# Performance work log

Measured on AMD Instinct MI355X. Metric: run time of the kernel, lower is better.

The kernel has to match this reference:

```python
import jax, jax.numpy as jnp
import numpy as np
from jax import lax

EPS = 1e-5

def binarize(x):
    # sign forward, straight-through (identity) backward, matching torch .data-trick Binarize
    return x + lax.stop_gradient(jnp.sign(x) - x)

def conv2d(x, w, pad):
    return lax.conv_general_dilated(x, w, window_strides=(1, 1),
                                    padding=[(pad, pad), (pad, pad)],
                                    dimension_numbers=('NCHW', 'OIHW', 'NCHW'))

def maxpool_k2s1(x):
    return lax.reduce_window(x, -jnp.inf, lax.max, (1, 1, 2, 2), (1, 1, 1, 1), 'VALID')

def batchnorm(x, g, b):
    # training-mode BN: batch statistics over (N, H, W)
    mean = jnp.mean(x, axis=(0, 2, 3), keepdims=True)
    var = jnp.var(x, axis=(0, 2, 3), keepdims=True)
    return (x - mean) * lax.rsqrt(var + EPS) * g[None, :, None, None] + b[None, :, None, None]

def hardtanh(x):
    return jnp.clip(x, -1.0, 1.0)

def setup_inputs() -> dict:
    key = jax.random.key(0)
    ks = jax.random.split(key, 11)
    B = 4096
    return {
        'x':   jax.random.normal(ks[0], (B, 12, 12, 15), jnp.float32),
        'w1':  jax.random.normal(ks[1], (48, 12, 3, 3), jnp.float32) * 0.1,
        'g1':  1.0 + 0.1 * jax.random.normal(ks[2], (48,), jnp.float32),
        'b1':  0.1 * jax.random.normal(ks[3], (48,), jnp.float32),
        'w2':  jax.random.normal(ks[4], (48, 48, 3, 3), jnp.float32) * 0.1,
        'g2':  1.0 + 0.1 * jax.random.normal(ks[5], (48,), jnp.float32),
        'b2':  0.1 * jax.random.normal(ks[6], (48,), jnp.float32),
        'w3':  jax.random.normal(ks[7], (48, 48, 3, 3), jnp.float32) * 0.1,
        'g3':  1.0 + 0.1 * jax.random.normal(ks[8], (48,), jnp.float32),
        'b3':  0.1 * jax.random.normal(ks[9], (48,), jnp.float32),
        'wfc': jax.random.normal(ks[10], (5, 54 * 48), jnp.float32) * 0.02,
    }

def reference(x, w1, g1, b1, w2, g2, b2, w3, g3, b3, wfc):
    # BinarizeConv2d binarizes activations (in_channels != 3) and weights; returns binarized input too
    xb1 = binarize(x)                                  # [B,12,12,15]
    h = conv2d(xb1, binarize(w1), pad=1)               # [B,48,12,15]
    h = maxpool_k2s1(h)                                # [B,48,11,14]
    h = hardtanh(batchnorm(h, g1, b1))
    xb2 = binarize(h)
    h = conv2d(xb2, binarize(w2), pad=0)               # [B,48,9,12]
    h = hardtanh(batchnorm(h, g2, b2))
    xb3 = binarize(h)
    h = conv2d(xb3, binarize(w3), pad=0)               # [B,48,7,10]
    h = maxpool_k2s1(h)                                # [B,48,6,9] -> 54 spatial
    h = hardtanh(batchnorm(h, g3, b3))
    f = h.reshape(h.shape[0], -1)                      # [B, 2592]
    fb = binarize(f)
    out = fb @ binarize(wfc).T                         # [B, 5]  (LogSoftmax defined but never applied)
    return (out, xb1, xb2, xb3, fb)
```

## Files before the change

### kernel.cpp

```cpp
#include <hip/hip_runtime.h>
#include <stdint.h>

typedef unsigned long long u64;
typedef unsigned short u16;


#define NB 4096

#define WS_STATS 0
#define WS_W1P   20480
#define WS_W2P   24576
#define WS_W3P   28672
#define WS_WFCP  32768
#define WS_A1    40960
#define WS_P1    5111808

#define OUT_OFF 0
#define XB1_OFF 20480
#define XB2_OFF 8867840
#define XB3_OFF 39145472
#define FB_OFF  60379136

__device__ __forceinline__ float fsign(float v) {
    return (v > 0.0f) ? 1.0f : ((v < 0.0f) ? -1.0f : 0.0f);
}

__global__ __launch_bounds__(512)
void kw_pack(const float* __restrict__ w1, const float* __restrict__ w2,
             const float* __restrict__ w3, const float* __restrict__ wfc,
             char* __restrict__ ws) {
    int t = threadIdx.x;
    long long* stats = (long long*)(ws + WS_STATS);
    for (int i = t; i < 2304; i += 512) stats[i] = 0;
    if (t < 432) {
        int oc = t / 9, p = t % 9;
        u16 m1 = 0;
        for (int c = 0; c < 12; ++c)
            if (w1[oc*108 + c*9 + p] > 0.0f) m1 |= (u16)(1u << c);
        ((u16*)(ws + WS_W1P))[t] = m1;
        u64 m2 = 0, m3 = 0;
        for (int c = 0; c < 48; ++c) {
            if (w2[oc*432 + c*9 + p] > 0.0f) m2 |= (1ull << c);
            if (w3[oc*432 + c*9 + p] > 0.0f) m3 |= (1ull << c);
        }
        ((u64*)(ws + WS_W2P))[t] = m2;
        ((u64*)(ws + WS_W3P))[t] = m3;
    }
    if (t < 205) {
        int o = t / 41, j = t % 41;
        u64 m = 0;
        for (int l = 0; l < 64; ++l) {
            int k = j*64 + l;
            if (k < 2592 && wfc[o*2592 + k] > 0.0f) m |= (1ull << l);
        }
        ((u64*)(ws + WS_WFCP))[t] = m;
    }
}

__global__ __launch_bounds__(256)
void k0_binx(const float* __restrict__ x, float* __restrict__ dout,
             char* __restrict__ ws) {
    int id = blockIdx.x*256 + threadIdx.x;
    int b = id / 45, s4 = id % 45;
    const float4* xp = (const float4*)(x + b*2160);
    float4* op = (float4*)(dout + XB1_OFF + (size_t)b*2160);
    u16 m0 = 0, m1 = 0, m2 = 0, m3 = 0;
    #pragma unroll
    for (int c = 0; c < 12; ++c) {
        float4 v = xp[c*45 + s4];
        float4 o;
        o.x = fsign(v.x); o.y = fsign(v.y); o.z = fsign(v.z); o.w = fsign(v.w);
        op[c*45 + s4] = o;
        u16 bit = (u16)(1u << c);
        if (v.x > 0.0f) m0 |= bit;
        if (v.y > 0.0f) m1 |= bit;
        if (v.z > 0.0f) m2 |= bit;
        if (v.w > 0.0f) m3 |= bit;
    }
    ushort4 mm; mm.x = m0; mm.y = m1; mm.z = m2; mm.w = m3;
    *((ushort4*)((u16*)(ws + WS_A1) + b*180 + s4*4)) = mm;
}

__global__ __launch_bounds__(256)
void k1_conv1(char* __restrict__ ws) {
    __shared__ u16 As[180];
    __shared__ u16 Wsh[432];
    __shared__ int cmap_i[2160];
    __shared__ int pl_i[1848];
    signed char* cmap = (signed char*)cmap_i;
    signed char* pl = (signed char*)pl_i;
    int t = threadIdx.x, b = blockIdx.x;
    const u16* A1 = (const u16*)(ws + WS_A1);
    const u16* W1p = (const u16*)(ws + WS_W1P);
    if (t < 180) As[t] = A1[b*180 + t];
    for (int i = t; i < 432; i += 256) Wsh[i] = W1p[i];
    __syncthreads();
    for (int i4 = t; i4 < 2160; i4 += 256) {
        int r = 0;
        #pragma unroll
        for (int u = 0; u < 4; ++u) {
            int i = i4*4 + u;
            int oc = i / 180, s = i % 180, y = s / 15, xx = s % 15;
            int acc = 0, valid = 0;
            #pragma unroll
            for (int ky = 0; ky < 3; ++ky) {
                int yy = y + ky - 1;
                if (yy < 0 || yy >= 12) continue;
                #pragma unroll
                for (int kx = 0; kx < 3; ++kx) {
                    int xc = xx + kx - 1;
                    if (xc < 0 || xc >= 15) continue;
                    acc += __popc((unsigned)(As[yy*15 + xc] ^ Wsh[oc*9 + ky*3 + kx]));
                    valid += 12;
                }
            }
            r |= ((valid - 2*acc) & 0xff) << (8*u);
        }
        cmap_i[i4] = r;
    }
    __syncthreads();
    int* gp = (int*)(ws + WS_P1 + (size_t)b*7392);
    for (int i4 = t; i4 < 1848; i4 += 256) {
        int r = 0;
        #pragma unroll
        for (int u = 0; u < 4; ++u) {
            int i = i4*4 + u;
            int c = i / 154, s = i % 154, py = s / 14, px = s % 14;
            int base = c*180 + py*15 + px;
            int mx = max(max((int)cmap[base],    (int)cmap[base+1]),
                         max((int)cmap[base+15], (int)cmap[base+16]));
            r |= (mx & 0xff) << (8*u);
        }
        pl_i[i4] = r;
        gp[i4] = r;
    }
    __syncthreads();
    int wv = t >> 6, ln = t & 63, slot = b & 7;
    u64* st = (u64*)(ws + WS_STATS);
    for (int c = wv; c < 48; c += 4) {
        int sum = 0, sq = 0;
        for (int s = ln; s < 154; s += 64) {
            int v = pl[c*154 + s];
            sum += v; sq += v*v;
        }
        #pragma unroll
        for (int off = 32; off >= 1; off >>= 1) {
            sum += __shfl_down(sum, off);
            sq  += __shfl_down(sq, off);
        }
        if (ln == 0) {
            atomicAdd(&st[(c)*8 + slot],      (u64)(long long)sum);
            atomicAdd(&st[(48 + c)*8 + slot], (u64)(long long)sq);
        }
    }
}

__global__ __launch_bounds__(256)
void kA_bn1conv2(const float* __restrict__ g1, const float* __restrict__ b1,
                 float* __restrict__ dout, char* __restrict__ ws) {
    __shared__ float sc[48], sh[48];
    __shared__ int sm_i[1848];
    __shared__ u64 As[154];
    __shared__ u64 Wsh[432];
    __shared__ short c2[5184];
    signed char* sm = (signed char*)sm_i;
    int t = threadIdx.x, b = blockIdx.x;
    const int* gp = (const int*)(ws + WS_P1 + (size_t)b*7392);
    for (int i4 = t; i4 < 1848; i4 += 256) sm_i[i4] = gp[i4];
    const u64* W2p = (const u64*)(ws + WS_W2P);
    for (int i = t; i < 432; i += 256) Wsh[i] = W2p[i];
    if (t < 48) {
        const long long* st = (const long long*)(ws + WS_STATS);
        long long s = 0, q = 0;
        #pragma unroll
        for (int k = 0; k < 8; ++k) { s += st[t*8 + k]; q += st[(48 + t)*8 + k]; }
        double N = 630784.0;
        double mean = (double)s / N;
        double var  = (double)q / N - mean*mean;
        double scale = (double)g1[t] / sqrt(var + 1e-5);
        sc[t] = (float)scale;
        sh[t] = (float)((double)b1[t] - mean*scale);
    }
    __syncthreads();
    float4* xo = (float4*)(dout + XB2_OFF + (size_t)b*7392);
    for (int i4 = t; i4 < 1848; i4 += 256) {
        int pv = sm_i[i4];
        int i = i4*4;
        float4 o;
        int c0 = i/154, c1 = (i+1)/154, c2i = (i+2)/154, c3 = (i+3)/154;
        o.x = fsign(sc[c0]*(float)(signed char)(pv)       + sh[c0]);
        o.y = fsign(sc[c1]*(float)(signed char)(pv >> 8)  + sh[c1]);
        o.z = fsign(sc[c2i]*(float)(signed char)(pv >> 16) + sh[c2i]);
        o.w = fsign(sc[c3]*(float)(signed char)(pv >> 24) + sh[c3]);
        xo[i4] = o;
    }
    if (t < 154) {
        u64 m = 0;
        #pragma unroll
        for (int c = 0; c < 48; ++c)
            if (sc[c]*(float)sm[c*154 + t] + sh[c] > 0.0f) m |= (1ull << c);
        As[t] = m;
        ((u64*)(ws + WS_A1))[(size_t)b*154 + t] = m;
    }
    __syncthreads();
    for (int i = t; i < 5184; i += 256) {
        int oc = i / 108, s = i % 108, oy = s / 12, ox = s % 12;
        int acc = 0;
        #pragma unroll
        for (int ky = 0; ky < 3; ++ky)
            #pragma unroll
            for (int kx = 0; kx < 3; ++kx)
                acc += __popcll(As[(oy+ky)*14 + ox+kx] ^ Wsh[oc*9 + ky*3 + kx]);
        c2[i] = (short)(432 - 2*acc);
    }
    __syncthreads();
    int wv = t >> 6, ln = t & 63, slot = b & 7;
    u64* st = (u64*)(ws + WS_STATS);
    for (int c = wv; c < 48; c += 4) {
        int sum = 0, sq = 0;
        for (int s = ln; s < 108; s += 64) {
            int v = c2[c*108 + s];
            sum += v; sq += v*v;
        }
        #pragma unroll
        for (int off = 32; off >= 1; off >>= 1) {
            sum += __shfl_down(sum, off);
            sq  += __shfl_down(sq, off);
        }
        if (ln == 0) {
            atomicAdd(&st[(96 + c)*8 + slot],  (u64)(long long)sum);
            atomicAdd(&st[(144 + c)*8 + slot], (u64)(long long)sq);
        }
    }
}

__global__ __launch_bounds__(256)
void kB_bn2conv3(const float* __restrict__ g2, const float* __restrict__ b2,
                 float* __restrict__ dout, char* __restrict__ ws) {
    __shared__ float sc[48], sh[48];
    __shared__ u64 As[154];
    __shared__ u64 W2s[432];
    __shared__ u64 W3s[432];
    __shared__ short c2[5184];
    __shared__ u64 A3[108];
    __shared__ short cm[3360];
    __shared__ short pl[2592];
    int t = threadIdx.x, b = blockIdx.x;
    if (t < 154) As[t] = ((const u64*)(ws + WS_A1))[(size_t)b*154 + t];
    const u64* W2p = (const u64*)(ws + WS_W2P);
    const u64* W3p = (const u64*)(ws + WS_W3P);
    for (int i = t; i < 432; i += 256) { W2s[i] = W2p[i]; W3s[i] = W3p[i]; }
    if (t < 48) {
        const long long* st = (const long long*)(ws + WS_STATS);
        long long s = 0, q = 0;
        #pragma unroll
        for (int k = 0; k < 8; ++k) { s += st[(96 + t)*8 + k]; q += st[(144 + t)*8 + k]; }
        double N = 442368.0;
        double mean = (double)s / N;
        double var  = (double)q / N - mean*mean;
        double scale = (double)g2[t] / sqrt(var + 1e-5);
        sc[t] = (float)scale;
        sh[t] = (float)((double)b2[t] - mean*scale);
    }
    __syncthreads();
    for (int i = t; i < 5184; i += 256) {
        int oc = i / 108, s = i % 108, oy = s / 12, ox = s % 12;
        int acc = 0;
        #pragma unroll
        for (int ky = 0; ky < 3; ++ky)
            #pragma unroll
            for (int kx = 0; kx < 3; ++kx)
                acc += __popcll(As[(oy+ky)*14 + ox+kx] ^ W2s[oc*9 + ky*3 + kx]);
        c2[i] = (short)(432 - 2*acc);
    }
    __syncthreads();
    float4* xo = (float4*)(dout + XB3_OFF + (size_t)b*5184);
    for (int i4 = t; i4 < 1296; i4 += 256) {
        int i = i4*4;
        float4 o;
        int c0 = i/108, c1 = (i+1)/108, c2i = (i+2)/108, c3 = (i+3)/108;
        o.x = fsign(sc[c0]*(float)c2[i]   + sh[c0]);
        o.y = fsign(sc[c1]*(float)c2[i+1] + sh[c1]);
        o.z = fsign(sc[c2i]*(float)c2[i+2] + sh[c2i]);
        o.w = fsign(sc[c3]*(float)c2[i+3] + sh[c3]);
        xo[i4] = o;
    }
    if (t < 108) {
        u64 m = 0;
        #pragma unroll
        for (int c = 0; c < 48; ++c)
            if (sc[c]*(float)c2[c*108 + t] + sh[c] > 0.0f) m |= (1ull << c);
        A3[t] = m;
    }
    __syncthreads();
    for (int i = t; i < 3360; i += 256) {
        int oc = i / 70, s = i % 70, oy = s / 10, ox = s % 10;
        int acc = 0;
        #pragma unroll
        for (int ky = 0; ky < 3; ++ky)
            #pragma unroll
            for (int kx = 0; kx < 3; ++kx)
                acc += __popcll(A3[(oy+ky)*12 + ox+kx] ^ W3s[oc*9 + ky*3 + kx]);
        cm[i] = (short)(432 - 2*acc);
    }
    __syncthreads();
    short* p3g = (short*)(ws + WS_P1) + (size_t)b*2592;
    for (int i = t; i < 2592; i += 256) {
        int c = i / 54, s = i % 54, py = s / 9, px = s % 9;
        int base = c*70 + py*10 + px;
        int mx = max(max((int)cm[base],    (int)cm[base+1]),
                     max((int)cm[base+10], (int)cm[base+11]));
        pl[i] = (short)mx;
        p3g[i] = (short)mx;
    }
    __syncthreads();
    int wv = t >> 6, ln = t & 63, slot = b & 7;
    u64* st = (u64*)(ws + WS_STATS);
    for (int c = wv; c < 48; c += 4) {
        int sum = 0, sq = 0;
        for (int s = ln; s < 54; s += 64) {
            int v = pl[c*54 + s];
            sum += v; sq += v*v;
        }
        #pragma unroll
        for (int off = 32; off >= 1; off >>= 1) {
            sum += __shfl_down(sum, off);
            sq  += __shfl_down(sq, off);
        }
        if (ln == 0) {
            atomicAdd(&st[(192 + c)*8 + slot], (u64)(long long)sum);
            atomicAdd(&st[(240 + c)*8 + slot], (u64)(long long)sq);
        }
    }
}

__global__ __launch_bounds__(256)
void kC_fbfc(const float* __restrict__ g3, const float* __restrict__ b3,
             float* __restrict__ dout, char* __restrict__ ws) {
    __shared__ float sc[48], sh[48];
    __shared__ short4 sm4[648];
    __shared__ unsigned char nib[648];
    __shared__ u64 fbb[41];
    short* sm = (short*)sm4;
    int t = threadIdx.x, b = blockIdx.x;
    const short4* p3 = (const short4*)((const short*)(ws + WS_P1) + (size_t)b*2592);
    for (int i4 = t; i4 < 648; i4 += 256) sm4[i4] = p3[i4];
    if (t < 48) {
        const long long* st = (const long long*)(ws + WS_STATS);
        long long s = 0, q = 0;
        #pragma unroll
        for (int k = 0; k < 8; ++k) { s += st[(192 + t)*8 + k]; q += st[(240 + t)*8 + k]; }
        double N = 221184.0;
        double mean = (double)s / N;
        double var  = (double)q / N - mean*mean;
        double scale = (double)g3[t] / sqrt(var + 1e-5);
        sc[t] = (float)scale;
        sh[t] = (float)((double)b3[t] - mean*scale);
    }
    __syncthreads();
    float4* fo = (float4*)(dout + FB_OFF + (size_t)b*2592);
    for (int i4 = t; i4 < 648; i4 += 256) {
        int i = i4*4;
        float4 o;
        unsigned n = 0;
        int c0 = i/54, c1 = (i+1)/54, c2 = (i+2)/54, c3 = (i+3)/54;
        float v0 = sc[c0]*(float)sm[i]   + sh[c0];
        float v1 = sc[c1]*(float)sm[i+1] + sh[c1];
        float v2 = sc[c2]*(float)sm[i+2] + sh[c2];
        float v3 = sc[c3]*(float)sm[i+3] + sh[c3];
        o.x = fsign(v0); o.y = fsign(v1); o.z = fsign(v2); o.w = fsign(v3);
        if (v0 > 0.0f) n |= 1u;
        if (v1 > 0.0f) n |= 2u;
        if (v2 > 0.0f) n |= 4u;
        if (v3 > 0.0f) n |= 8u;
        fo[i4] = o;
        nib[i4] = (unsigned char)n;
    }
    __syncthreads();
    if (t < 41) {
        u64 m = 0;
        #pragma unroll
        for (int k = 0; k < 16; ++k) {
            int j = t*16 + k;
            if (j < 648) m |= ((u64)nib[j]) << (4*k);
        }
        fbb[t] = m;
    }
    __syncthreads();
    if (t < 5) {
        const u64* Wf = (const u64*)(ws + WS_WFCP) + t*41;
        int acc = 0;
        #pragma unroll
        for (int j = 0; j < 41; ++j) acc += __popcll(fbb[j] ^ Wf[j]);
        dout[OUT_OFF + b*5 + t] = (float)(2592 - 2*acc);
    }
}

extern "C" void kernel_launch(void* const* d_in, const int* in_sizes, int n_in,
                              void* d_out, int out_size, void* d_ws, size_t ws_size,
                              hipStream_t stream) {
    const float* x   = (const float*)d_in[0];
    const float* w1  = (const float*)d_in[1];
    const float* g1  = (const float*)d_in[2];
    const float* b1  = (const float*)d_in[3];
    const float* w2  = (const float*)d_in[4];
    const float* g2  = (const float*)d_in[5];
    const float* b2  = (const float*)d_in[6];
    const float* w3  = (const float*)d_in[7];
    const float* g3  = (const float*)d_in[8];
    const float* b3  = (const float*)d_in[9];
    const float* wfc = (const float*)d_in[10];
    float* out = (float*)d_out;
    char* ws = (char*)d_ws;

    hipLaunchKernelGGL(kw_pack,     dim3(1),    dim3(512), 0, stream, w1, w2, w3, wfc, ws);
    hipLaunchKernelGGL(k0_binx,     dim3(720),  dim3(256), 0, stream, x, out, ws);
    hipLaunchKernelGGL(k1_conv1,    dim3(NB),   dim3(256), 0, stream, ws);
    hipLaunchKernelGGL(kA_bn1conv2, dim3(NB),   dim3(256), 0, stream, g1, b1, out, ws);
    hipLaunchKernelGGL(kB_bn2conv3, dim3(NB),   dim3(256), 0, stream, g2, b2, out, ws);
    hipLaunchKernelGGL(kC_fbfc,     dim3(NB),   dim3(256), 0, stream, g3, b3, out, ws);
}
```

Baseline: 734.6 us.

## Restructure binary convs so each thread holds its taps and loops over output channels

The three popcount convolutions now give each thread one output pixel. The thread loads its 9 input taps into registers once and loops over all 48 output channels, reading weights straight from global memory (uniform, cacheable) instead of staging them in shared memory. Block sizes shrink to 192/128 threads to match the pixel counts, and the xb3 write uses per-channel short4 loads. This cuts repeated shared-memory tap reads and divisions and frees LDS for occupancy, but fewer threads per block work serially through 48 channels and rely on scalar and global loads for weights.

```diff
diff --git a/kernel.cpp b/kernel.cpp
--- a/kernel.cpp
+++ b/kernel.cpp
@@ -81,63 +81,54 @@
     *((ushort4*)((u16*)(ws + WS_A1) + b*180 + s4*4)) = mm;
 }
 
-__global__ __launch_bounds__(256)
+__global__ __launch_bounds__(192)
 void k1_conv1(char* __restrict__ ws) {
     __shared__ u16 As[180];
-    __shared__ u16 Wsh[432];
-    __shared__ int cmap_i[2160];
-    __shared__ int pl_i[1848];
-    signed char* cmap = (signed char*)cmap_i;
-    signed char* pl = (signed char*)pl_i;
+    __shared__ signed char cmap[8640];
+    __shared__ signed char pl[7392];
     int t = threadIdx.x, b = blockIdx.x;
-    const u16* A1 = (const u16*)(ws + WS_A1);
-    const u16* W1p = (const u16*)(ws + WS_W1P);
-    if (t < 180) As[t] = A1[b*180 + t];
-    for (int i = t; i < 432; i += 256) Wsh[i] = W1p[i];
-    __syncthreads();
-    for (int i4 = t; i4 < 2160; i4 += 256) {
-        int r = 0;
-        #pragma unroll
-        for (int u = 0; u < 4; ++u) {
-            int i = i4*4 + u;
-            int oc = i / 180, s = i % 180, y = s / 15, xx = s % 15;
-            int acc = 0, valid = 0;
-            #pragma unroll
-            for (int ky = 0; ky < 3; ++ky) {
-                int yy = y + ky - 1;
-                if (yy < 0 || yy >= 12) continue;
-                #pragma unroll
-                for (int kx = 0; kx < 3; ++kx) {
-                    int xc = xx + kx - 1;
-                    if (xc < 0 || xc >= 15) continue;
-                    acc += __popc((unsigned)(As[yy*15 + xc] ^ Wsh[oc*9 + ky*3 + kx]));
-                    valid += 12;
-                }
+    const u16* A1 = (const u16*)(ws + WS_A1) + b*180;
+    if (t < 180) As[t] = A1[t];
+    const u16* __restrict__ W1g = (const u16*)(ws + WS_W1P);
+    __syncthreads();
+    if (t < 180) {
+        int y = t / 15, xx = t % 15;
+        u16 tap[9], msk[9];
+        int nv = 0;
+        #pragma unroll
+        for (int ky = 0; ky < 3; ++ky) {
+            #pragma unroll
+            for (int kx = 0; kx < 3; ++kx) {
+                int yy = y + ky - 1, xc = xx + kx - 1;
+                bool v = (yy >= 0 && yy < 12 && xc >= 0 && xc < 15);
+                int yl = min(max(yy, 0), 11), xl = min(max(xc, 0), 14);
+                tap[ky*3+kx] = As[yl*15 + xl];
+                msk[ky*3+kx] = v ? (u16)0xFFFF : (u16)0;
+                nv += v ? 12 : 0;
             }
-            r |= ((valid - 2*acc) & 0xff) << (8*u);
-        }
-        cmap_i[i4] = r;
-    }
-    __syncthreads();
-    int* gp = (int*)(ws + WS_P1 + (size_t)b*7392);
-    for (int i4 = t; i4 < 1848; i4 += 256) {
-        int r = 0;
-        #pragma unroll
-        for (int u = 0; u < 4; ++u) {
-            int i = i4*4 + u;
-            int c = i / 154, s = i % 154, py = s / 14, px = s % 14;
-            int base = c*180 + py*15 + px;
-            int mx = max(max((int)cmap[base],    (int)cmap[base+1]),
-                         max((int)cmap[base+15], (int)cmap[base+16]));
-            r |= (mx & 0xff) << (8*u);
-        }
-        pl_i[i4] = r;
-        gp[i4] = r;
+        }
+        for (int oc = 0; oc < 48; ++oc) {
+            int acc = 0;
+            #pragma unroll
+            for (int k = 0; k < 9; ++k)
+                acc += __popc((unsigned)((u16)(tap[k] ^ W1g[oc*9 + k]) & msk[k]));
+            cmap[oc*180 + t] = (signed char)(nv - 2*acc);
+        }
+    }
+    __syncthreads();
+    signed char* gp = (signed char*)(ws + WS_P1) + (size_t)b*7392;
+    for (int i = t; i < 7392; i += 192) {
+        int c = i / 154, s = i % 154, py = s / 14, px = s % 14;
+        int base = c*180 + py*15 + px;
+        int mx = max(max((int)cmap[base],    (int)cmap[base+1]),
+                     max((int)cmap[base+15], (int)cmap[base+16]));
+        pl[i] = (signed char)mx;
+        gp[i] = (signed char)mx;
     }
     __syncthreads();
     int wv = t >> 6, ln = t & 63, slot = b & 7;
     u64* st = (u64*)(ws + WS_STATS);
-    for (int c = wv; c < 48; c += 4) {
+    for (int c = wv; c < 48; c += 3) {
         int sum = 0, sq = 0;
         for (int s = ln; s < 154; s += 64) {
             int v = pl[c*154 + s];
@@ -149,26 +140,24 @@
             sq  += __shfl_down(sq, off);
         }
         if (ln == 0) {
-            atomicAdd(&st[(c)*8 + slot],      (u64)(long long)sum);
+            atomicAdd(&st[c*8 + slot],        (u64)(long long)sum);
             atomicAdd(&st[(48 + c)*8 + slot], (u64)(long long)sq);
         }
     }
 }
 
-__global__ __launch_bounds__(256)
+__global__ __launch_bounds__(128)
 void kA_bn1conv2(const float* __restrict__ g1, const float* __restrict__ b1,
                  float* __restrict__ dout, char* __restrict__ ws) {
     __shared__ float sc[48], sh[48];
     __shared__ int sm_i[1848];
     __shared__ u64 As[154];
-    __shared__ u64 Wsh[432];
-    __shared__ short c2[5184];
+    __shared__ short c2s[5184];
     signed char* sm = (signed char*)sm_i;
     int t = threadIdx.x, b = blockIdx.x;
     const int* gp = (const int*)(ws + WS_P1 + (size_t)b*7392);
-    for (int i4 = t; i4 < 1848; i4 += 256) sm_i[i4] = gp[i4];
-    const u64* W2p = (const u64*)(ws + WS_W2P);
-    for (int i = t; i < 432; i += 256) Wsh[i] = W2p[i];
+    for (int i4 = t; i4 < 1848; i4 += 128) sm_i[i4] = gp[i4];
+    const u64* __restrict__ W2g = (const u64*)(ws + WS_W2P);
     if (t < 48) {
         const long long* st = (const long long*)(ws + WS_STATS);
         long long s = 0, q = 0;
@@ -183,43 +172,50 @@
     }
     __syncthreads();
     float4* xo = (float4*)(dout + XB2_OFF + (size_t)b*7392);
-    for (int i4 = t; i4 < 1848; i4 += 256) {
+    for (int i4 = t; i4 < 1848; i4 += 128) {
         int pv = sm_i[i4];
         int i = i4*4;
         float4 o;
         int c0 = i/154, c1 = (i+1)/154, c2i = (i+2)/154, c3 = (i+3)/154;
-        o.x = fsign(sc[c0]*(float)(signed char)(pv)       + sh[c0]);
-        o.y = fsign(sc[c1]*(float)(signed char)(pv >> 8)  + sh[c1]);
+        o.x = fsign(sc[c0]*(float)(signed char)(pv)        + sh[c0]);
+        o.y = fsign(sc[c1]*(float)(signed char)(pv >> 8)   + sh[c1]);
         o.z = fsign(sc[c2i]*(float)(signed char)(pv >> 16) + sh[c2i]);
-        o.w = fsign(sc[c3]*(float)(signed char)(pv >> 24) + sh[c3]);
+        o.w = fsign(sc[c3]*(float)(signed char)(pv >> 24)  + sh[c3]);
         xo[i4] = o;
     }
-    if (t < 154) {
+    u64* A2g = (u64*)(ws + WS_A1) + (size_t)b*154;
+    for (int s = t; s < 154; s += 128) {
         u64 m = 0;
         #pragma unroll
         for (int c = 0; c < 48; ++c)
-            if (sc[c]*(float)sm[c*154 + t] + sh[c] > 0.0f) m |= (1ull << c);
-        As[t] = m;
-        ((u64*)(ws + WS_A1))[(size_t)b*154 + t] = m;
-    }
-    __syncthreads();
-    for (int i = t; i < 5184; i += 256) {
-        int oc = i / 108, s = i % 108, oy = s / 12, ox = s % 12;
-        int acc = 0;
+            if (sc[c]*(float)sm[c*154 + s] + sh[c] > 0.0f) m |= (1ull << c);
+        As[s] = m;
+        A2g[s] = m;
+    }
+    __syncthreads();
+    if (t < 108) {
+        int oy = t / 12, ox = t % 12;
+        u64 tap[9];
         #pragma unroll
         for (int ky = 0; ky < 3; ++ky)
             #pragma unroll
             for (int kx = 0; kx < 3; ++kx)
-                acc += __popcll(As[(oy+ky)*14 + ox+kx] ^ Wsh[oc*9 + ky*3 + kx]);
-        c2[i] = (short)(432 - 2*acc);
+                tap[ky*3+kx] = As[(oy+ky)*14 + ox + kx];
+        for (int oc = 0; oc < 48; ++oc) {
+            int acc = 0;
+            #pragma unroll
+            for (int k = 0; k < 9; ++k)
+                acc += __popcll(tap[k] ^ W2g[oc*9 + k]);
+            c2s[oc*108 + t] = (short)(432 - 2*acc);
+        }
     }
     __syncthreads();
     int wv = t >> 6, ln = t & 63, slot = b & 7;
     u64* st = (u64*)(ws + WS_STATS);
-    for (int c = wv; c < 48; c += 4) {
+    for (int c = wv; c < 48; c += 2) {
         int sum = 0, sq = 0;
         for (int s = ln; s < 108; s += 64) {
-            int v = c2[c*108 + s];
+            int v = c2s[c*108 + s];
             sum += v; sq += v*v;
         }
         #pragma unroll
@@ -234,22 +230,20 @@
     }
 }
 
-__global__ __launch_bounds__(256)
+__global__ __launch_bounds__(128)
 void kB_bn2conv3(const float* __restrict__ g2, const float* __restrict__ b2,
                  float* __restrict__ dout, char* __restrict__ ws) {
     __shared__ float sc[48], sh[48];
     __shared__ u64 As[154];
-    __shared__ u64 W2s[432];
-    __shared__ u64 W3s[432];
-    __shared__ short c2[5184];
+    __shared__ short c2s[5184];
     __shared__ u64 A3[108];
     __shared__ short cm[3360];
-    __shared__ short pl[2592];
+    __shared__ short pls[2592];
     int t = threadIdx.x, b = blockIdx.x;
-    if (t < 154) As[t] = ((const u64*)(ws + WS_A1))[(size_t)b*154 + t];
-    const u64* W2p = (const u64*)(ws + WS_W2P);
-    const u64* W3p = (const u64*)(ws + WS_W3P);
-    for (int i = t; i < 432; i += 256) { W2s[i] = W2p[i]; W3s[i] = W3p[i]; }
+    const u64* A2g = (const u64*)(ws + WS_A1) + (size_t)b*154;
+    for (int s = t; s < 154; s += 128) As[s] = A2g[s];
+    const u64* __restrict__ W2g = (const u64*)(ws + WS_W2P);
+    const u64* __restrict__ W3g = (const u64*)(ws + WS_W3P);
     if (t < 48) {
         const long long* st = (const long long*)(ws + WS_STATS);
         long long s = 0, q = 0;
@@ -263,64 +257,76 @@
         sh[t] = (float)((double)b2[t] - mean*scale);
     }
     __syncthreads();
-    for (int i = t; i < 5184; i += 256) {
-        int oc = i / 108, s = i % 108, oy = s / 12, ox = s % 12;
-        int acc = 0;
+    if (t < 108) {
+        int oy = t / 12, ox = t % 12;
+        u64 tap[9];
         #pragma unroll
         for (int ky = 0; ky < 3; ++ky)
             #pragma unroll
             for (int kx = 0; kx < 3; ++kx)
-                acc += __popcll(As[(oy+ky)*14 + ox+kx] ^ W2s[oc*9 + ky*3 + kx]);
-        c2[i] = (short)(432 - 2*acc);
+                tap[ky*3+kx] = As[(oy+ky)*14 + ox + kx];
+        for (int oc = 0; oc < 48; ++oc) {
+            int acc = 0;
+            #pragma unroll
+            for (int k = 0; k < 9; ++k)
+                acc += __popcll(tap[k] ^ W2g[oc*9 + k]);
+            c2s[oc*108 + t] = (short)(432 - 2*acc);
+        }
     }
     __syncthreads();
     float4* xo = (float4*)(dout + XB3_OFF + (size_t)b*5184);
-    for (int i4 = t; i4 < 1296; i4 += 256) {
-        int i = i4*4;
+    for (int i4 = t; i4 < 1296; i4 += 128) {
+        int c = i4 / 27, s4 = i4 % 27;
+        short4 v4 = *(const short4*)&c2s[c*108 + s4*4];
         float4 o;
-        int c0 = i/108, c1 = (i+1)/108, c2i = (i+2)/108, c3 = (i+3)/108;
-        o.x = fsign(sc[c0]*(float)c2[i]   + sh[c0]);
-        o.y = fsign(sc[c1]*(float)c2[i+1] + sh[c1]);
-        o.z = fsign(sc[c2i]*(float)c2[i+2] + sh[c2i]);
-        o.w = fsign(sc[c3]*(float)c2[i+3] + sh[c3]);
+        o.x = fsign(sc[c]*(float)v4.x + sh[c]);
+        o.y = fsign(sc[c]*(float)v4.y + sh[c]);
+        o.z = fsign(sc[c]*(float)v4.z + sh[c]);
+        o.w = fsign(sc[c]*(float)v4.w + sh[c]);
         xo[i4] = o;
     }
     if (t < 108) {
         u64 m = 0;
         #pragma unroll
         for (int c = 0; c < 48; ++c)
-            if (sc[c]*(float)c2[c*108 + t] + sh[c] > 0.0f) m |= (1ull << c);
+            if (sc[c]*(float)c2s[c*108 + t] + sh[c] > 0.0f) m |= (1ull << c);
         A3[t] = m;
     }
     __syncthreads();
-    for (int i = t; i < 3360; i += 256) {
-        int oc = i / 70, s = i % 70, oy = s / 10, ox = s % 10;
-        int acc = 0;
+    if (t < 70) {
+        int oy = t / 10, ox = t % 10;
+        u64 tap[9];
         #pragma unroll
         for (int ky = 0; ky < 3; ++ky)
             #pragma unroll
             for (int kx = 0; kx < 3; ++kx)
-                acc += __popcll(A3[(oy+ky)*12 + ox+kx] ^ W3s[oc*9 + ky*3 + kx]);
-        cm[i] = (short)(432 - 2*acc);
+                tap[ky*3+kx] = A3[(oy+ky)*12 + ox + kx];
+        for (int oc = 0; oc < 48; ++oc) {
+            int acc = 0;
+            #pragma unroll
+            for (int k = 0; k < 9; ++k)
+                acc += __popcll(tap[k] ^ W3g[oc*9 + k]);
+            cm[oc*70 + t] = (short)(432 - 2*acc);
+        }
     }
     __syncthreads();
     short* p3g = (short*)(ws + WS_P1) + (size_t)b*2592;
-    for (int i = t; i < 2592; i += 256) {
+    for (int i = t; i < 2592; i += 128) {
         int c = i / 54, s = i % 54, py = s / 9, px = s % 9;
         int base = c*70 + py*10 + px;
         int mx = max(max((int)cm[base],    (int)cm[base+1]),
                      max((int)cm[base+10], (int)cm[base+11]));
-        pl[i] = (short)mx;
+        pls[i] = (short)mx;
         p3g[i] = (short)mx;
     }
     __syncthreads();
     int wv = t >> 6, ln = t & 63, slot = b & 7;
     u64* st = (u64*)(ws + WS_STATS);
-    for (int c = wv; c < 48; c += 4) {
+    for (int c = wv; c < 48; c += 2) {
         int sum = 0, sq = 0;
-        for (int s = ln; s < 54; s += 64) {
-            int v = pl[c*54 + s];
-            sum += v; sq += v*v;
+        if (ln < 54) {
+            int v = pls[c*54 + ln];
+            sum = v; sq = v*v;
         }
         #pragma unroll
         for (int off = 32; off >= 1; off >>= 1) {
@@ -415,8 +421,8 @@
 
     hipLaunchKernelGGL(kw_pack,     dim3(1),    dim3(512), 0, stream, w1, w2, w3, wfc, ws);
     hipLaunchKernelGGL(k0_binx,     dim3(720),  dim3(256), 0, stream, x, out, ws);
-    hipLaunchKernelGGL(k1_conv1,    dim3(NB),   dim3(256), 0, stream, ws);
-    hipLaunchKernelGGL(kA_bn1conv2, dim3(NB),   dim3(256), 0, stream, g1, b1, out, ws);
-    hipLaunchKernelGGL(kB_bn2conv3, dim3(NB),   dim3(256), 0, stream, g2, b2, out, ws);
+    hipLaunchKernelGGL(k1_conv1,    dim3(NB),   dim3(192), 0, stream, ws);
+    hipLaunchKernelGGL(kA_bn1conv2, dim3(NB),   dim3(128), 0, stream, g1, b1, out, ws);
+    hipLaunchKernelGGL(kB_bn2conv3, dim3(NB),   dim3(128), 0, stream, g2, b2, out, ws);
     hipLaunchKernelGGL(kC_fbfc,     dim3(NB),   dim3(256), 0, stream, g3, b3, out, ws);
 }
```

New measurement: 768.5 us. 1.05x slower.
